# Optimization experiments

Measured on AMD Instinct MI355X. Metric: run time of the kernel, lower is better.

## Reference

```python
import jax, jax.numpy as jnp
import numpy as np

B, T, D, H = 2, 2048, 1024, 16
HD = D // H  # 64


def _rotary_tables(t, hd):
    # standard RoPE cos/sin tables, shape [T, hd]
    inv_freq = 1.0 / (10000.0 ** (jnp.arange(0, hd, 2, dtype=jnp.float32) / hd))
    freqs = jnp.arange(t, dtype=jnp.float32)[:, None] * inv_freq[None, :]  # [T, hd/2]
    emb = jnp.concatenate([freqs, freqs], axis=-1)  # [T, hd]
    return jnp.cos(emb), jnp.sin(emb)


def setup_inputs() -> dict:
    key = jax.random.key(0)
    kx, kq, kk, kv, kp = jax.random.split(key, 5)
    x = jax.random.normal(kx, (B, T, D), dtype=jnp.float32)
    cos_t, sin_t = _rotary_tables(T, HD)
    cos = jnp.broadcast_to(cos_t[None], (B, T, HD)).astype(jnp.float32)
    sin = jnp.broadcast_to(sin_t[None], (B, T, HD)).astype(jnp.float32)
    scale = 0.02
    Wq = jax.random.normal(kq, (D, D), dtype=jnp.float32) * scale
    Wk = jax.random.normal(kk, (D, D), dtype=jnp.float32) * scale
    Wv = jax.random.normal(kv, (D, D), dtype=jnp.float32) * scale
    Wp = jax.random.normal(kp, (D, D), dtype=jnp.float32) * scale
    return {"x": x, "cos": cos, "sin": sin, "Wq": Wq, "Wk": Wk, "Wv": Wv, "Wp": Wp}


def _rotate_half(x):
    x1, x2 = jnp.split(x, 2, axis=-1)
    return jnp.concatenate([-x2, x1], axis=-1)


def reference(x, cos, sin, Wq, Wk, Wv, Wp):
    b, t, d = x.shape
    h, hd = H, HD
    # torch Linear: y = x @ W.T
    q = jnp.einsum('btd,ed->bte', x, Wq).reshape(b, t, h, hd)
    k = jnp.einsum('btd,ed->bte', x, Wk).reshape(b, t, h, hd)
    v = jnp.einsum('btd,ed->bte', x, Wv).reshape(b, t, h, hd)
    # RoPE, cos/sin [B,T,hd] -> broadcast over heads (unsqueeze_dim=2)
    c = cos[:, :, None, :]
    s = sin[:, :, None, :]
    q = q * c + _rotate_half(q) * s
    k = k * c + _rotate_half(k) * s
    # causal attention, softmax scale = 1/sqrt(head_dim) (flash_attn default)
    scale = 1.0 / np.sqrt(hd).astype(np.float32)
    scores = jnp.einsum('bqhd,bkhd->bhqk', q, k) * scale  # [B,H,T,T]
    mask = jnp.tril(jnp.ones((t, t), dtype=bool))
    scores = jnp.where(mask[None, None], scores, jnp.finfo(scores.dtype).min)
    probs = jax.nn.softmax(scores, axis=-1)
    out = jnp.einsum('bhqk,bkhd->bqhd', probs, v).reshape(b, t, d)
    return jnp.einsum('btd,ed->bte', out, Wp)
```

## Files before the change

### kernel.cpp

```cpp
#include <hip/hip_runtime.h>
#include <hip/hip_bf16.h>

typedef __attribute__((ext_vector_type(8))) short bf16x8s;
typedef __attribute__((ext_vector_type(4))) float f32x4;
typedef __attribute__((ext_vector_type(16))) float f32x16;
typedef __attribute__((ext_vector_type(4))) __bf16 bf16x4;
typedef __attribute__((ext_vector_type(8))) __bf16 bf16x8;

typedef const __attribute__((address_space(1))) void gvoid_t;
typedef __attribute__((address_space(3))) void lvoid_t;

constexpr int Bc = 2, Tc = 2048, Dc = 1024, Hc = 16, HDc = 64;
constexpr int Mc = Bc * Tc;

__global__ void cvt_all(const float* __restrict__ x,
                        const float* __restrict__ wq, const float* __restrict__ wk,
                        const float* __restrict__ wv, const float* __restrict__ wp,
                        __bf16* __restrict__ xb, __bf16* __restrict__ wb) {
  const int bid = blockIdx.x;
  const float* src;
  __bf16* dst;
  int i;
  if (bid < 4096) {
    src = x; dst = xb; i = (bid * 256 + threadIdx.x) * 4;
  } else {
    const int r = bid - 4096;
    const int w = r >> 10;
    src = (w == 0) ? wq : (w == 1) ? wk : (w == 2) ? wv : wp;
    dst = wb + (size_t)w * (Dc * Dc);
    i = ((r & 1023) * 256 + threadIdx.x) * 4;
  }
  float4 v = *(const float4*)(src + i);
  bf16x4 o;
  o[0] = (__bf16)v.x; o[1] = (__bf16)v.y; o[2] = (__bf16)v.z; o[3] = (__bf16)v.w;
  *(bf16x4*)(dst + i) = o;
}

__launch_bounds__(512, 2)
__global__ void gemm_qkv(const __bf16* __restrict__ A,
                         const __bf16* __restrict__ W,
                         __bf16* __restrict__ outb,
                         __bf16* __restrict__ vtout,
                         const float* __restrict__ cbt,
                         const float* __restrict__ sbt) {
  __shared__ __bf16 Abuf[4][128 * 32];
  __shared__ __bf16 Bbuf[4][3][128 * 32];
  const int tid = threadIdx.x;
  const int lane = tid & 63, wid = tid >> 6;
  const int wr = wid >> 1, wc = wid & 1;
  const int lr = lane & 15, lg = lane >> 4;
  const int lid = blockIdx.x + 8 * blockIdx.y;
  const int xcd = lid & 7, g = lid >> 3;
  const int brow = (xcd * 4 + (g & 3)) * 128;
  const int bcol = (g >> 2) * 128;

  f32x4 acc[3][2][4] = {};

  const char* Ag = (const char*)(A + (size_t)brow * Dc);
  const char* Bg = (const char*)(W + (size_t)bcol * Dc);
  const int rp = tid >> 3;
  const int unswz = (tid & 7) ^ (rp & 7);
  const int srow = 2 * rp + (unswz >> 2);
  const int skoff = (unswz & 3) * 16;

#define STAGE(K0, BUF)                                                                    \
  do {                                                                                    \
    __builtin_amdgcn_global_load_lds(                                                     \
        (gvoid_t*)(Ag + (size_t)srow * (Dc * 2) + (K0)*2 + skoff),                        \
        (lvoid_t*)((char*)Abuf[BUF] + tid * 16), 16, 0, 0);                               \
    _Pragma("unroll")                                                                     \
    for (int z_ = 0; z_ < 3; ++z_)                                                        \
      __builtin_amdgcn_global_load_lds(                                                   \
          (gvoid_t*)(Bg + (size_t)z_ * (Dc * Dc * 2) + (size_t)srow * (Dc * 2) +          \
                     (K0)*2 + skoff),                                                     \
          (lvoid_t*)((char*)Bbuf[BUF][z_] + tid * 16), 16, 0, 0);                         \
  } while (0)

  STAGE(0, 0);
  STAGE(32, 1);

  const int swb = ((((lr & 1) << 2) | lg) ^ (lr >> 1)) << 4;
  const int lrh = lr >> 1;

  for (int s = 0; s < 32; ++s) {
    if (s + 2 < 32) {
      STAGE((s + 2) * 32, (s + 2) & 3);
      asm volatile("s_waitcnt vmcnt(8)" ::: "memory");
    } else if (s + 1 < 32) {
      asm volatile("s_waitcnt vmcnt(4)" ::: "memory");
    } else {
      asm volatile("s_waitcnt vmcnt(0)" ::: "memory");
    }
    __builtin_amdgcn_sched_barrier(0);
    __builtin_amdgcn_s_barrier();
    __builtin_amdgcn_sched_barrier(0);

    const char* Al = (const char*)Abuf[s & 3];
    const char* Bl0 = (const char*)Bbuf[s & 3][0];
    bf16x8s af[2];
#pragma unroll
    for (int m = 0; m < 2; ++m)
      af[m] = *(const bf16x8s*)(Al + (wr * 16 + m * 8 + lrh) * 128 + swb);
#pragma unroll
    for (int z = 0; z < 3; ++z) {
      const char* Bl = Bl0 + z * (128 * 32 * 2);
      bf16x8s bfv[4];
#pragma unroll
      for (int n = 0; n < 4; ++n)
        bfv[n] = *(const bf16x8s*)(Bl + (wc * 32 + n * 8 + lrh) * 128 + swb);
      __builtin_amdgcn_s_setprio(1);
#pragma unroll
      for (int m = 0; m < 2; ++m)
#pragma unroll
        for (int n = 0; n < 4; ++n)
          acc[z][m][n] =
              __builtin_amdgcn_mfma_f32_16x16x32_bf16(af[m], bfv[n], acc[z][m][n], 0, 0, 0);
      __builtin_amdgcn_s_setprio(0);
    }
  }
#undef STAGE

  const int h = (bcol >> 6) + wc;
#pragma unroll
  for (int z = 0; z < 2; ++z) {
    const float scl = (z == 0) ? 0.18033688011112042f : 1.0f;
    __bf16* dst = outb + (size_t)z * ((size_t)Mc * Dc);
#pragma unroll
    for (int m = 0; m < 2; ++m) {
#pragma unroll
      for (int j = 0; j < 4; ++j) {
        const int gm = brow + wr * 32 + m * 16 + lg * 4 + j;
        const int bb = gm >> 11, t = gm & (Tc - 1);
        const float* cbase = cbt + (size_t)gm * HDc;
        const float* sbase = sbt + (size_t)gm * HDc;
#pragma unroll
        for (int n = 0; n < 2; ++n) {
          const int i = n * 16 + lr;
          const float c0 = cbase[i], s0 = sbase[i];
          const float v0 = acc[z][m][n][j], v1 = acc[z][m][n + 2][j];
          acc[z][m][n][j]     = (v0 * c0 - v1 * s0) * scl;
          acc[z][m][n + 2][j] = (v1 * c0 + v0 * s0) * scl;
        }
        __bf16* rowp = dst + (((size_t)bb * Hc + h) * Tc + t) * HDc;
#pragma unroll
        for (int n = 0; n < 4; ++n) rowp[n * 16 + lr] = (__bf16)acc[z][m][n][j];
      }
    }
  }

  {
    const int bb2 = brow >> 11, t0b = brow & (Tc - 1);
    __bf16* tile_t = (__bf16*)Abuf;
#pragma unroll
    for (int h2 = 0; h2 < 2; ++h2) {
      __syncthreads();
      if (wc == h2) {
#pragma unroll
        for (int n = 0; n < 4; ++n)
#pragma unroll
          for (int m = 0; m < 2; ++m)
#pragma unroll
            for (int j = 0; j < 4; ++j)
              tile_t[(n * 16 + lr) * 136 + wr * 32 + m * 16 + lg * 4 + j] =
                  (__bf16)acc[2][m][n][j];
      }
      __syncthreads();
      const int hh2 = (bcol >> 6) + h2;
#pragma unroll
      for (int p = 0; p < 2; ++p) {
        const int r = p * 32 + (tid >> 4);
        const int c8 = (tid & 15) * 8;
        bf16x8 vvv = *(const bf16x8*)(tile_t + r * 136 + c8);
        *(bf16x8*)(vtout + (((size_t)bb2 * Hc + hh2) * HDc + r) * Tc + t0b + c8) = vvv;
      }
    }
  }
}

__launch_bounds__(256, 2)
__global__ void gemm_proj(const __bf16* __restrict__ A, const __bf16* __restrict__ W,
                          float* __restrict__ outf) {
  __shared__ __bf16 Alds[128 * 64];
  __shared__ __bf16 Blds[64 * 64];
  const int tid = threadIdx.x;
  const int lane = tid & 63, wid = tid >> 6;
  const int lr = lane & 15, lg = lane >> 4;
  const int lid = blockIdx.x + (int)gridDim.x * blockIdx.y;
  const int xcd = lid & 7, g = lid >> 3;
  const int brow = (xcd * 4 + (g & 3)) * 128;
  const int bcol = (g >> 2) * 64;
  f32x4 acc[2][4] = {};
  const char* Ag = (const char*)(A + (size_t)brow * Dc);
  const char* Bg = (const char*)(W + (size_t)bcol * Dc);
  const int r0 = tid >> 3;
  const int cb = (tid & 7) * 16;
  for (int k0 = 0; k0 < Dc; k0 += 64) {
#pragma unroll
    for (int i = 0; i < 4; ++i) {
      const int r = i * 32 + r0;
      const int ldsoff = (i * 256 + wid * 64) * 16;
      __builtin_amdgcn_global_load_lds(
          (gvoid_t*)(Ag + (size_t)r * (Dc * 2) + k0 * 2 + cb),
          (lvoid_t*)((char*)Alds + ldsoff), 16, 0, 0);
    }
#pragma unroll
    for (int i = 0; i < 2; ++i) {
      const int r = i * 32 + r0;
      const int ldsoff = (i * 256 + wid * 64) * 16;
      __builtin_amdgcn_global_load_lds(
          (gvoid_t*)(Bg + (size_t)r * (Dc * 2) + k0 * 2 + cb),
          (lvoid_t*)((char*)Blds + ldsoff), 16, 0, 0);
    }
    __syncthreads();
#pragma unroll
    for (int kk = 0; kk < 2; ++kk) {
      const int col = kk * 32 + lg * 8;
      bf16x8s af[2], bfv[4];
#pragma unroll
      for (int m = 0; m < 2; ++m)
        af[m] = *(const bf16x8s*)(Alds + (wid * 32 + m * 16 + lr) * 64 + col);
#pragma unroll
      for (int n = 0; n < 4; ++n)
        bfv[n] = *(const bf16x8s*)(Blds + (n * 16 + lr) * 64 + col);
#pragma unroll
      for (int m = 0; m < 2; ++m)
#pragma unroll
        for (int n = 0; n < 4; ++n)
          acc[m][n] = __builtin_amdgcn_mfma_f32_16x16x32_bf16(bfv[n], af[m], acc[m][n], 0, 0, 0);
    }
    __syncthreads();
  }
#pragma unroll
  for (int m = 0; m < 2; ++m) {
    const int gm = brow + wid * 32 + m * 16 + lr;
    float* rowp = outf + (size_t)gm * Dc + bcol;
#pragma unroll
    for (int n = 0; n < 4; ++n) {
      float4 fv;
      fv.x = acc[m][n][0]; fv.y = acc[m][n][1]; fv.z = acc[m][n][2]; fv.w = acc[m][n][3];
      *(float4*)(rowp + n * 16 + lg * 4) = fv;
    }
  }
}

__launch_bounds__(512, 4)
__global__ void attn_kernel(const __bf16* __restrict__ Q, const __bf16* __restrict__ K,
                            const __bf16* __restrict__ Vt, __bf16* __restrict__ O) {
  __shared__ __bf16 Klds[2][128 * 64];
  __shared__ __bf16 Vlds[2][64 * 128];
  const int f = blockIdx.x;
  const int xcd = f & 7, g = f >> 3;
  const int pass = g >> 4, g4 = g & 15;
  const int bh = xcd * 4 + pass;
  const int qt = ((pass >> 1) & 1) ? (15 - g4) : g4;
  const int tid = threadIdx.x;
  const int lane = tid & 63, wid = tid >> 6;
  const int qq = wid >> 1, kp = wid & 1;
  const int q31 = lane & 31, hh = lane >> 5;
  const int k3 = q31 & 7;
  const int v15 = q31 & 15;
  const __bf16* Qp = Q + (size_t)bh * Tc * HDc;
  const char* Kb = (const char*)(K + (size_t)bh * Tc * HDc);
  const char* Vb = (const char*)(Vt + (size_t)bh * HDc * Tc);

  const int units = qt + 1;

  const int sr = tid >> 3;
  const int sxor = ((tid & 7) ^ (sr & 7)) << 4;
  const int vr = tid >> 4;
  const int vxor = ((tid & 15) ^ (vr & 15)) << 4;
  const char* vsrc = Vb + (size_t)vr * (Tc * 2) + vxor;

  const int q0w = qt * 128 + qq * 32;
  bf16x8s qf[4];
#pragma unroll
  for (int ks = 0; ks < 4; ++ks)
    qf[ks] = *(const bf16x8s*)(Qp + (q0w + q31) * HDc + ks * 16 + hh * 8);

  const int b = bh >> 4, h = bh & 15;

  f32x16 acc0 = {}, acc1 = {};
  float lsum = 0.f;

#define STAGE(IT, BUF)                                                                   \
  do {                                                                                   \
    _Pragma("unroll")                                                                    \
    for (int i_ = 0; i_ < 2; ++i_) {                                                     \
      __builtin_amdgcn_global_load_lds(                                                  \
          (gvoid_t*)(Kb + (size_t)((IT) * 128 + i_ * 64 + sr) * 128 + sxor),             \
          (lvoid_t*)((char*)Klds[BUF] + i_ * 8192 + wid * 1024), 16, 0, 0);              \
      __builtin_amdgcn_global_load_lds(                                                  \
          (gvoid_t*)(vsrc + (size_t)i_ * 32 * (Tc * 2) + (IT) * 256),                    \
          (lvoid_t*)((char*)Vlds[BUF] + i_ * 8192 + wid * 1024), 16, 0, 0);              \
    }                                                                                    \
  } while (0)

  STAGE(0, 0);
  asm volatile("s_waitcnt vmcnt(0)" ::: "memory");
  __builtin_amdgcn_sched_barrier(0);
  __builtin_amdgcn_s_barrier();
  __builtin_amdgcn_sched_barrier(0);

  for (int u = 0; u < units; ++u) {
    if (u + 1 < units) STAGE(u + 1, (u + 1) & 1);
    __builtin_amdgcn_sched_barrier(0);

    const bool last = (u == qt);
    if (!(last && kp == 1 && qq < 2)) {
      const char* Kl = (const char*)Klds[u & 1];
      const char* Vl = (const char*)Vlds[u & 1];
      const bool fin = last && ((qq >> 1) == kp);
      const int thr = q0w + q31 - u * 128 - kp * 64 - 4 * hh;

#pragma unroll
      for (int ct = 0; ct < 2; ++ct) {
        bf16x8s kf[4];
#pragma unroll
        for (int ks = 0; ks < 4; ++ks)
          kf[ks] = *(const bf16x8s*)(Kl + (kp * 64 + ct * 32 + q31) * 128 +
                                     (((2 * ks + hh) ^ k3) << 4));
        f32x16 z = {};
        __builtin_amdgcn_s_setprio(1);
#pragma unroll
        for (int ks = 0; ks < 4; ++ks)
          z = __builtin_amdgcn_mfma_f32_32x32x16_bf16(kf[ks], qf[ks], z, 0, 0, 0);
        __builtin_amdgcn_s_setprio(0);

        unsigned w0[4], w1[4];
#pragma unroll
        for (int n = 0; n < 4; ++n) {
          float e[4];
#pragma unroll
          for (int j = 0; j < 4; ++j) {
            float ev = __builtin_amdgcn_exp2f(z[n * 4 + j]);
            if (fin && (ct * 32 + n * 8 + j > thr)) ev = 0.f;
            lsum += ev;
            e[j] = ev;
          }
          asm("v_cvt_pk_bf16_f32 %0, %1, %2" : "=v"(w0[n]) : "v"(e[0]), "v"(e[1]));
          asm("v_cvt_pk_bf16_f32 %0, %1, %2" : "=v"(w1[n]) : "v"(e[2]), "v"(e[3]));
        }

        bf16x8s pfr[2];
#pragma unroll
        for (int ks2 = 0; ks2 < 2; ++ks2) {
          unsigned a = w0[2 * ks2], bb2 = w0[2 * ks2 + 1];
          unsigned c = w1[2 * ks2], d = w1[2 * ks2 + 1];
          asm volatile("v_permlane32_swap_b32 %0, %1" : "+v"(a), "+v"(bb2));
          asm volatile("v_permlane32_swap_b32 %0, %1" : "+v"(c), "+v"(d));
          union { unsigned u[4]; bf16x8s v; } uu;
          uu.u[0] = a; uu.u[1] = c; uu.u[2] = bb2; uu.u[3] = d;
          pfr[ks2] = uu.v;
        }

        __builtin_amdgcn_s_setprio(1);
#pragma unroll
        for (int ks2 = 0; ks2 < 2; ++ks2) {
          const int so = ((kp * 8 + ct * 4 + 2 * ks2 + hh) ^ v15) << 4;
          const bf16x8s va0 = *(const bf16x8s*)(Vl + q31 * 256 + so);
          const bf16x8s va1 = *(const bf16x8s*)(Vl + (32 + q31) * 256 + so);
          acc0 = __builtin_amdgcn_mfma_f32_32x32x16_bf16(va0, pfr[ks2], acc0, 0, 0, 0);
          acc1 = __builtin_amdgcn_mfma_f32_32x32x16_bf16(va1, pfr[ks2], acc1, 0, 0, 0);
        }
        __builtin_amdgcn_s_setprio(0);
      }
    }

    if (u + 1 < units) {
      asm volatile("s_waitcnt vmcnt(0)" ::: "memory");
      __builtin_amdgcn_sched_barrier(0);
      __builtin_amdgcn_s_barrier();
      __builtin_amdgcn_sched_barrier(0);
    }
  }
#undef STAGE

  __syncthreads();
  float* kscr = (float*)&Klds[0][0];
  float* lscr = (float*)&Vlds[0][0];
  if (kp == 1) {
#pragma unroll
    for (int i = 0; i < 16; ++i) {
      kscr[qq * 2048 + i * 64 + lane] = acc0[i];
      kscr[qq * 2048 + 1024 + i * 64 + lane] = acc1[i];
    }
    lscr[qq * 64 + lane] = lsum;
  }
  __syncthreads();
  if (kp == 0) {
#pragma unroll
    for (int i = 0; i < 16; ++i) {
      acc0[i] += kscr[qq * 2048 + i * 64 + lane];
      acc1[i] += kscr[qq * 2048 + 1024 + i * 64 + lane];
    }
    lsum += lscr[qq * 64 + lane];
    const float lt = lsum + __shfl_xor(lsum, 32);
    const float linv = 1.f / lt;
    const int t = q0w + q31;
    __bf16* dst = O + ((size_t)b * Tc + t) * Dc + h * HDc;
#pragma unroll
    for (int qd = 0; qd < 4; ++qd) {
      bf16x4 o0, o1;
#pragma unroll
      for (int j = 0; j < 4; ++j) {
        o0[j] = (__bf16)(acc0[qd * 4 + j] * linv);
        o1[j] = (__bf16)(acc1[qd * 4 + j] * linv);
      }
      *(bf16x4*)(dst + qd * 8 + hh * 4) = o0;
      *(bf16x4*)(dst + 32 + qd * 8 + hh * 4) = o1;
    }
  }
}

extern "C" void kernel_launch(void* const* d_in, const int* in_sizes, int n_in,
                              void* d_out, int out_size, void* d_ws, size_t ws_size,
                              hipStream_t stream) {
  const float* x   = (const float*)d_in[0];
  const float* cbt = (const float*)d_in[1];
  const float* sbt = (const float*)d_in[2];
  const float* Wq  = (const float*)d_in[3];
  const float* Wk  = (const float*)d_in[4];
  const float* Wv  = (const float*)d_in[5];
  const float* Wp  = (const float*)d_in[6];
  float* out = (float*)d_out;
  char* ws = (char*)d_ws;
  __bf16* xb = (__bf16*)(ws);
  __bf16* wb = (__bf16*)(ws + (8u << 20));
  __bf16* qb = (__bf16*)(ws + (16u << 20));
  __bf16* vt = (__bf16*)(ws + (40u << 20));
  __bf16* ao = (__bf16*)(ws + (48u << 20));
  __bf16* kb = qb + (size_t)Mc * Dc;

  cvt_all<<<8192, 256, 0, stream>>>(x, Wq, Wk, Wv, Wp, xb, wb);
  gemm_qkv<<<dim3(8, 32), 512, 0, stream>>>(xb, wb, qb, vt, cbt, sbt);
  attn_kernel<<<512, 512, 0, stream>>>(qb, kb, vt, ao);
  gemm_proj<<<dim3(16, 32), 256, 0, stream>>>(ao, wb + 3u * (Dc * Dc), out);
}
```

Measured before the change: 92.98 us.

## Shrink QKV GEMM tile to 64x128 with 256 threads and double buffering

Restructures the fused QKV GEMM from 512-thread 128x128 tiles with a 4-deep, 2-ahead LDS pipeline to 256-thread 64-row by 128-column tiles with a 2-buffer, 1-ahead pipeline. The grid doubles to 512 blocks and drops the XCD-aware remapping, which should improve occupancy and load balance across CUs. It adds an extra barrier per K step and reduces prefetch depth, which may expose memory latency. The V-transpose epilogue is also merged into a single pass.

```diff
diff --git a/kernel.cpp b/kernel.cpp
--- a/kernel.cpp
+++ b/kernel.cpp
@@ -36,23 +36,23 @@
   *(bf16x4*)(dst + i) = o;
 }
 
-__launch_bounds__(512, 2)
+__launch_bounds__(256, 2)
 __global__ void gemm_qkv(const __bf16* __restrict__ A,
                          const __bf16* __restrict__ W,
                          __bf16* __restrict__ outb,
                          __bf16* __restrict__ vtout,
                          const float* __restrict__ cbt,
                          const float* __restrict__ sbt) {
-  __shared__ __bf16 Abuf[4][128 * 32];
-  __shared__ __bf16 Bbuf[4][3][128 * 32];
+  __shared__ char smem[57344];
+  char* Abase = smem;
+  char* Bbase = smem + 8192;
   const int tid = threadIdx.x;
   const int lane = tid & 63, wid = tid >> 6;
   const int wr = wid >> 1, wc = wid & 1;
   const int lr = lane & 15, lg = lane >> 4;
   const int lid = blockIdx.x + 8 * blockIdx.y;
-  const int xcd = lid & 7, g = lid >> 3;
-  const int brow = (xcd * 4 + (g & 3)) * 128;
-  const int bcol = (g >> 2) * 128;
+  const int bcol = (lid & 7) * 128;
+  const int brow = (lid >> 3) * 64;
 
   f32x4 acc[3][2][4] = {};
 
@@ -60,34 +60,36 @@
   const char* Bg = (const char*)(W + (size_t)bcol * Dc);
   const int rp = tid >> 3;
   const int unswz = (tid & 7) ^ (rp & 7);
-  const int srow = 2 * rp + (unswz >> 2);
+  const int srow0 = 2 * rp + (unswz >> 2);
   const int skoff = (unswz & 3) * 16;
 
 #define STAGE(K0, BUF)                                                                    \
   do {                                                                                    \
     __builtin_amdgcn_global_load_lds(                                                     \
-        (gvoid_t*)(Ag + (size_t)srow * (Dc * 2) + (K0)*2 + skoff),                        \
-        (lvoid_t*)((char*)Abuf[BUF] + tid * 16), 16, 0, 0);                               \
+        (gvoid_t*)(Ag + (size_t)srow0 * (Dc * 2) + (K0)*2 + skoff),                       \
+        (lvoid_t*)(Abase + (BUF)*4096 + tid * 16), 16, 0, 0);                             \
     _Pragma("unroll")                                                                     \
-    for (int z_ = 0; z_ < 3; ++z_)                                                        \
+    for (int z_ = 0; z_ < 3; ++z_) {                                                      \
+      const char* bz_ = Bg + (size_t)z_ * (Dc * Dc * 2) + (K0)*2 + skoff;                 \
+      char* bl_ = Bbase + ((BUF)*3 + z_) * 8192;                                          \
       __builtin_amdgcn_global_load_lds(                                                   \
-          (gvoid_t*)(Bg + (size_t)z_ * (Dc * Dc * 2) + (size_t)srow * (Dc * 2) +          \
-                     (K0)*2 + skoff),                                                     \
-          (lvoid_t*)((char*)Bbuf[BUF][z_] + tid * 16), 16, 0, 0);                         \
+          (gvoid_t*)(bz_ + (size_t)srow0 * (Dc * 2)),                                     \
+          (lvoid_t*)(bl_ + tid * 16), 16, 0, 0);                                          \
+      __builtin_amdgcn_global_load_lds(                                                   \
+          (gvoid_t*)(bz_ + (size_t)(srow0 + 64) * (Dc * 2)),                              \
+          (lvoid_t*)(bl_ + 4096 + tid * 16), 16, 0, 0);                                   \
+    }                                                                                     \
   } while (0)
 
   STAGE(0, 0);
-  STAGE(32, 1);
 
   const int swb = ((((lr & 1) << 2) | lg) ^ (lr >> 1)) << 4;
   const int lrh = lr >> 1;
 
   for (int s = 0; s < 32; ++s) {
-    if (s + 2 < 32) {
-      STAGE((s + 2) * 32, (s + 2) & 3);
-      asm volatile("s_waitcnt vmcnt(8)" ::: "memory");
-    } else if (s + 1 < 32) {
-      asm volatile("s_waitcnt vmcnt(4)" ::: "memory");
+    if (s + 1 < 32) {
+      STAGE((s + 1) * 32, (s + 1) & 1);
+      asm volatile("s_waitcnt vmcnt(7)" ::: "memory");
     } else {
       asm volatile("s_waitcnt vmcnt(0)" ::: "memory");
     }
@@ -95,15 +97,15 @@
     __builtin_amdgcn_s_barrier();
     __builtin_amdgcn_sched_barrier(0);
 
-    const char* Al = (const char*)Abuf[s & 3];
-    const char* Bl0 = (const char*)Bbuf[s & 3][0];
+    const char* Al = Abase + (s & 1) * 4096;
+    const char* Bl0 = Bbase + (s & 1) * 3 * 8192;
     bf16x8s af[2];
 #pragma unroll
     for (int m = 0; m < 2; ++m)
       af[m] = *(const bf16x8s*)(Al + (wr * 16 + m * 8 + lrh) * 128 + swb);
 #pragma unroll
     for (int z = 0; z < 3; ++z) {
-      const char* Bl = Bl0 + z * (128 * 32 * 2);
+      const char* Bl = Bl0 + z * 8192;
       bf16x8s bfv[4];
 #pragma unroll
       for (int n = 0; n < 4; ++n)
@@ -117,6 +119,9 @@
               __builtin_amdgcn_mfma_f32_16x16x32_bf16(af[m], bfv[n], acc[z][m][n], 0, 0, 0);
       __builtin_amdgcn_s_setprio(0);
     }
+    __builtin_amdgcn_sched_barrier(0);
+    __builtin_amdgcn_s_barrier();
+    __builtin_amdgcn_sched_barrier(0);
   }
 #undef STAGE
 
@@ -150,29 +155,24 @@
 
   {
     const int bb2 = brow >> 11, t0b = brow & (Tc - 1);
-    __bf16* tile_t = (__bf16*)Abuf;
-#pragma unroll
-    for (int h2 = 0; h2 < 2; ++h2) {
-      __syncthreads();
-      if (wc == h2) {
-#pragma unroll
-        for (int n = 0; n < 4; ++n)
-#pragma unroll
-          for (int m = 0; m < 2; ++m)
-#pragma unroll
-            for (int j = 0; j < 4; ++j)
-              tile_t[(n * 16 + lr) * 136 + wr * 32 + m * 16 + lg * 4 + j] =
-                  (__bf16)acc[2][m][n][j];
-      }
-      __syncthreads();
-      const int hh2 = (bcol >> 6) + h2;
-#pragma unroll
-      for (int p = 0; p < 2; ++p) {
-        const int r = p * 32 + (tid >> 4);
-        const int c8 = (tid & 15) * 8;
-        bf16x8 vvv = *(const bf16x8*)(tile_t + r * 136 + c8);
-        *(bf16x8*)(vtout + (((size_t)bb2 * Hc + hh2) * HDc + r) * Tc + t0b + c8) = vvv;
-      }
+    __bf16* tile_t = (__bf16*)smem;
+#pragma unroll
+    for (int m = 0; m < 2; ++m)
+#pragma unroll
+      for (int n = 0; n < 4; ++n)
+#pragma unroll
+        for (int j = 0; j < 4; ++j)
+          tile_t[(wc * 64 + n * 16 + lr) * 72 + wr * 32 + m * 16 + lg * 4 + j] =
+              (__bf16)acc[2][m][n][j];
+    __syncthreads();
+#pragma unroll
+    for (int p = 0; p < 4; ++p) {
+      const int r = p * 32 + (tid >> 3);
+      const int c8 = (tid & 7) * 8;
+      bf16x8 vvv = *(const bf16x8*)(tile_t + r * 72 + c8);
+      const int gn = bcol + r;
+      const int hh2 = gn >> 6, hd = gn & 63;
+      *(bf16x8*)(vtout + (((size_t)bb2 * Hc + hh2) * HDc + hd) * Tc + t0b + c8) = vvv;
     }
   }
 }
@@ -432,7 +432,7 @@
   __bf16* kb = qb + (size_t)Mc * Dc;
 
   cvt_all<<<8192, 256, 0, stream>>>(x, Wq, Wk, Wv, Wp, xb, wb);
-  gemm_qkv<<<dim3(8, 32), 512, 0, stream>>>(xb, wb, qb, vt, cbt, sbt);
+  gemm_qkv<<<dim3(8, 64), 256, 0, stream>>>(xb, wb, qb, vt, cbt, sbt);
   attn_kernel<<<512, 512, 0, stream>>>(qb, kb, vt, ao);
   gemm_proj<<<dim3(16, 32), 256, 0, stream>>>(ao, wb + 3u * (Dc * Dc), out);
 }
```

New measurement: 100.5 us. 8.1% more time.
